# Kernel optimization log

Hardware: AMD Instinct MI355X
Metric: run time of the kernel (lower is better)

## Reference

```python
import jax, jax.numpy as jnp
import numpy as np


def setup_inputs() -> dict:
    key = jax.random.key(0)
    k1, k2, k3 = jax.random.split(key, 3)
    B, N, F = 32, 1024, 128
    x = jax.random.normal(k1, (B, N, F), dtype=jnp.float32)
    adj = jax.random.uniform(k2, (B, N, N), dtype=jnp.float32)
    # Linear(in_feature=128, out_feature=128) params (Kaiming-ish scale)
    W = jax.random.normal(k3, (F, F), dtype=jnp.float32) * (1.0 / np.sqrt(F))
    b = jnp.zeros((F,), dtype=jnp.float32)
    return {"x": x, "adj": adj, "W": W, "b": b}


def reference(x, adj, W, b):
    # h = W(x) ; dropout is identity in inference mode
    h = jnp.einsum("bnf,fg->bng", x, W) + b          # [B,N,F]
    h = jnp.einsum("bnm,bmf->bnf", adj, h)           # neighbor aggregation
    return jax.nn.relu(h + x)                          # residual + ReLU
```

## Files before the change

kernel.cpp:

```cpp
#include <hip/hip_runtime.h>
#include <stdint.h>

typedef unsigned short u16;
typedef __attribute__((ext_vector_type(4))) u16    u16x4;
typedef __attribute__((ext_vector_type(8))) u16    u16x8;
typedef __attribute__((ext_vector_type(4))) float  f32x4;
typedef __attribute__((ext_vector_type(8))) __bf16 bf16x8;

__device__ __forceinline__ u16 f2bf(float f) {
    union { float f; uint32_t u; } v; v.f = f;
    uint32_t u = v.u;
    uint32_t rb = 0x7FFFu + ((u >> 16) & 1u);
    return (u16)((u + rb) >> 16);
}

__global__ __launch_bounds__(256) void gcn_wt(const float* __restrict__ W,
                                              u16* __restrict__ Wt) {
    int idx = blockIdx.x * 256 + threadIdx.x;
    int k = idx >> 7, f = idx & 127;
    Wt[f * 128 + k] = f2bf(W[idx]);
}

__global__ __launch_bounds__(256) void gcn_xw(const float* __restrict__ x,
                                              const u16* __restrict__ Wt,
                                              const float* __restrict__ bias,
                                              u16* __restrict__ hT) {
    __shared__ u16 Wl[128 * 128];
    __shared__ u16 Xl[128 * 128];
    const int t  = threadIdx.x;
    const int bb = blockIdx.x >> 3;
    const int n0 = (blockIdx.x & 7) << 7;

#pragma unroll
    for (int i = 0; i < 16; ++i) {
        int o  = i * 256 + t;
        int f  = o >> 5;
        int kb = (o & 31) * 8;
        u16x4 v = *(const u16x4*)((const char*)Wt + o * 8);
        *(u16x4*)((char*)Wl + f * 256 + (kb ^ ((f & 7) << 4))) = v;
    }
    const float* xb = x + (size_t)bb * (1024 * 128) + (size_t)n0 * 128;
#pragma unroll
    for (int i = 0; i < 16; ++i) {
        int o4 = i * 256 + t;
        int n  = o4 >> 5;
        int kb = (o4 & 31) * 8;
        f32x4 v = *(const f32x4*)(xb + (size_t)o4 * 4);
        u16x4 h; h.x = f2bf(v.x); h.y = f2bf(v.y); h.z = f2bf(v.z); h.w = f2bf(v.w);
        *(u16x4*)((char*)Xl + n * 256 + (kb ^ ((n & 7) << 4))) = h;
    }
    __syncthreads();

    const int w = t >> 6, l = t & 63;
    const int wr = w >> 1, wc = w & 1;
    f32x4 acc[4][4] = {};
#pragma unroll
    for (int kk = 0; kk < 4; ++kk) {
        const int kbyte = kk * 64 + (l >> 4) * 16;
        bf16x8 a[4], b[4];
#pragma unroll
        for (int mf = 0; mf < 4; ++mf) {
            int fl = wr * 64 + mf * 16 + (l & 15);
            a[mf] = *(const bf16x8*)((const char*)Wl + fl * 256 + (kbyte ^ ((fl & 7) << 4)));
        }
#pragma unroll
        for (int nn = 0; nn < 4; ++nn) {
            int nl = wc * 64 + nn * 16 + (l & 15);
            b[nn] = *(const bf16x8*)((const char*)Xl + nl * 256 + (kbyte ^ ((nl & 7) << 4)));
        }
#pragma unroll
        for (int mf = 0; mf < 4; ++mf)
#pragma unroll
            for (int nn = 0; nn < 4; ++nn)
                acc[mf][nn] = __builtin_amdgcn_mfma_f32_16x16x32_bf16(
                    a[mf], b[nn], acc[mf][nn], 0, 0, 0);
    }

    u16* ho = hT + (size_t)bb * 131072;
#pragma unroll
    for (int mf = 0; mf < 4; ++mf) {
        int fbase = wr * 64 + mf * 16 + (l >> 4) * 4;
#pragma unroll
        for (int r = 0; r < 4; ++r) {
            float bv = bias[fbase + r];
#pragma unroll
            for (int nn = 0; nn < 4; ++nn) {
                int n = wc * 64 + nn * 16 + (l & 15);
                ho[(size_t)(fbase + r) * 1024 + n0 + n] = f2bf(acc[mf][nn][r] + bv);
            }
        }
    }
}

__global__ __launch_bounds__(256) void gcn_agg(const float* __restrict__ adj,
                                               const u16* __restrict__ hT,
                                               const float* __restrict__ x,
                                               float* __restrict__ out) {
    __shared__ u16 Al[64 * 64];
    __shared__ u16 Bl[128 * 64];

    const int t = threadIdx.x;
    const int L  = (blockIdx.x & 7) * 64 + (blockIdx.x >> 3);
    const int bb = L >> 4;
    const int r0 = (L & 15) << 6;

    const float* adjb = adj + (size_t)bb * 1024 * 1024 + (size_t)r0 * 1024;
    const u16*   hTb  = hT + (size_t)bb * 131072;

    const int w = t >> 6, l = t & 63;
    const int wr = w >> 1, wc = w & 1;
    f32x4 acc[2][4] = {};

    f32x4 aReg[4];
    u16x8 bReg[4];
#pragma unroll
    for (int i = 0; i < 4; ++i) {
        int o4 = i * 256 + t;
        aReg[i] = *(const f32x4*)(adjb + (size_t)(o4 >> 4) * 1024 + (o4 & 15) * 4);
        int o16 = i * 256 + t;
        bReg[i] = *(const u16x8*)((const char*)(hTb + (size_t)(o16 >> 3) * 1024) + (o16 & 7) * 16);
    }

    for (int ks = 0; ks < 16; ++ks) {
        if (ks) __syncthreads();
#pragma unroll
        for (int i = 0; i < 4; ++i) {
            int o4 = i * 256 + t;
            int r = o4 >> 4, kb = (o4 & 15) * 8;
            u16x4 h; h.x = f2bf(aReg[i].x); h.y = f2bf(aReg[i].y);
            h.z = f2bf(aReg[i].z); h.w = f2bf(aReg[i].w);
            *(u16x4*)((char*)Al + r * 128 + (kb ^ ((r & 7) << 4))) = h;
            int o16 = i * 256 + t;
            int f = o16 >> 3, kb2 = (o16 & 7) * 16;
            *(u16x8*)((char*)Bl + f * 128 + (kb2 ^ ((f & 7) << 4))) = bReg[i];
        }
        __syncthreads();

        if (ks + 1 < 16) {
            int k0n = (ks + 1) * 64;
#pragma unroll
            for (int i = 0; i < 4; ++i) {
                int o4 = i * 256 + t;
                aReg[i] = *(const f32x4*)(adjb + (size_t)(o4 >> 4) * 1024 + k0n + (o4 & 15) * 4);
                int o16 = i * 256 + t;
                bReg[i] = *(const u16x8*)((const char*)(hTb + (size_t)(o16 >> 3) * 1024 + k0n) + (o16 & 7) * 16);
            }
        }

#pragma unroll
        for (int kk = 0; kk < 2; ++kk) {
            const int kbyte = kk * 64 + (l >> 4) * 16;
            bf16x8 a[2], b[4];
#pragma unroll
            for (int mf = 0; mf < 2; ++mf) {
                int rl = wr * 32 + mf * 16 + (l & 15);
                a[mf] = *(const bf16x8*)((const char*)Al + rl * 128 + (kbyte ^ ((rl & 7) << 4)));
            }
#pragma unroll
            for (int nn = 0; nn < 4; ++nn) {
                int fl = wc * 64 + nn * 16 + (l & 15);
                b[nn] = *(const bf16x8*)((const char*)Bl + fl * 128 + (kbyte ^ ((fl & 7) << 4)));
            }
#pragma unroll
            for (int mf = 0; mf < 2; ++mf)
#pragma unroll
                for (int nn = 0; nn < 4; ++nn)
                    acc[mf][nn] = __builtin_amdgcn_mfma_f32_16x16x32_bf16(
                        a[mf], b[nn], acc[mf][nn], 0, 0, 0);
        }
    }

    const float* xb = x + (size_t)bb * 131072;
    float*       ob = out + (size_t)bb * 131072;
#pragma unroll
    for (int mf = 0; mf < 2; ++mf) {
#pragma unroll
        for (int j = 0; j < 4; ++j) {
            int r = r0 + wr * 32 + mf * 16 + (l >> 4) * 4 + j;
#pragma unroll
            for (int nn = 0; nn < 4; ++nn) {
                int f = wc * 64 + nn * 16 + (l & 15);
                size_t idx = (size_t)r * 128 + f;
                float v = acc[mf][nn][j] + xb[idx];
                ob[idx] = fmaxf(v, 0.0f);
            }
        }
    }
}

extern "C" void kernel_launch(void* const* d_in, const int* in_sizes, int n_in,
                              void* d_out, int out_size, void* d_ws, size_t ws_size,
                              hipStream_t stream) {
    const float* x    = (const float*)d_in[0];
    const float* adj  = (const float*)d_in[1];
    const float* W    = (const float*)d_in[2];
    const float* bias = (const float*)d_in[3];
    float* out = (float*)d_out;

    u16* hT = (u16*)d_ws;
    u16* Wt = (u16*)((char*)d_ws + (size_t)32 * 131072 * 2);

    gcn_wt <<<dim3(64),  dim3(256), 0, stream>>>(W, Wt);
    gcn_xw <<<dim3(256), dim3(256), 0, stream>>>(x, Wt, bias, hT);
    gcn_agg<<<dim3(512), dim3(256), 0, stream>>>(adj, hT, x, out);
}
```

Before: 40.54 us.

## Stream adj and hT directly to LDS with double-buffered async loads

The aggregation kernel now uses global_load_lds to copy fp32 adjacency tiles and bf16 hT tiles straight into double-buffered shared memory, using a pre-swizzled source addressing scheme. The fp32-to-bf16 conversion moves from the staging path to the fragment read just before the MFMA. This removes the register round trip and lets the next tile's load overlap compute. The cost is doubled LDS (fp32 adj tile plus two buffers), which may reduce occupancy, and conversion work is repeated per wave read.

```diff
diff --git a/kernel.cpp b/kernel.cpp
--- a/kernel.cpp
+++ b/kernel.cpp
@@ -12,6 +12,13 @@
     uint32_t u = v.u;
     uint32_t rb = 0x7FFFu + ((u >> 16) & 1u);
     return (u16)((u + rb) >> 16);
+}
+
+__device__ __forceinline__ bf16x8 cvt8(f32x4 a, f32x4 b) {
+    bf16x8 r;
+    r[0] = (__bf16)a.x; r[1] = (__bf16)a.y; r[2] = (__bf16)a.z; r[3] = (__bf16)a.w;
+    r[4] = (__bf16)b.x; r[5] = (__bf16)b.y; r[6] = (__bf16)b.z; r[7] = (__bf16)b.w;
+    return r;
 }
 
 __global__ __launch_bounds__(256) void gcn_wt(const float* __restrict__ W,
@@ -96,79 +103,91 @@
                                                const u16* __restrict__ hT,
                                                const float* __restrict__ x,
                                                float* __restrict__ out) {
-    __shared__ u16 Al[64 * 64];
-    __shared__ u16 Bl[128 * 64];
+    __shared__ float Al[2][64 * 64];
+    __shared__ u16   Bl[2][128 * 64];
 
     const int t = threadIdx.x;
     const int L  = (blockIdx.x & 7) * 64 + (blockIdx.x >> 3);
     const int bb = L >> 4;
     const int r0 = (L & 15) << 6;
 
-    const float* adjb = adj + (size_t)bb * 1024 * 1024 + (size_t)r0 * 1024;
+    const float* adjb = adj + (size_t)bb * 1048576 + (size_t)r0 * 1024;
     const u16*   hTb  = hT + (size_t)bb * 131072;
 
     const int w = t >> 6, l = t & 63;
     const int wr = w >> 1, wc = w & 1;
+
+    const float* srcA[4];
+    const u16*   srcB[4];
+#pragma unroll
+    for (int i = 0; i < 4; ++i) {
+        int c  = (w * 4 + i) * 64 + l;
+        int rA = c >> 4, cbA = ((c & 15) * 16) ^ ((rA & 7) << 4);
+        srcA[i] = adjb + (size_t)rA * 1024 + (cbA >> 2);
+        int fB = c >> 3, cbB = ((c & 7) * 16) ^ ((fB & 7) << 4);
+        srcB[i] = hTb + (size_t)fB * 1024 + (cbB >> 1);
+    }
+
+#define STAGE(buf, ks)                                                          \
+    do {                                                                        \
+        const int k0 = (ks) * 64;                                               \
+        _Pragma("unroll")                                                       \
+        for (int i = 0; i < 4; ++i) {                                           \
+            __builtin_amdgcn_global_load_lds(                                   \
+                (const __attribute__((address_space(1))) void*)(srcA[i] + k0),  \
+                (__attribute__((address_space(3))) void*)((char*)&Al[buf][0] + (w * 4 + i) * 1024), \
+                16, 0, 0);                                                      \
+            __builtin_amdgcn_global_load_lds(                                   \
+                (const __attribute__((address_space(1))) void*)(srcB[i] + k0),  \
+                (__attribute__((address_space(3))) void*)((char*)&Bl[buf][0] + (w * 4 + i) * 1024), \
+                16, 0, 0);                                                      \
+        }                                                                       \
+    } while (0)
+
+#define COMPUTE(buf)                                                            \
+    do {                                                                        \
+        _Pragma("unroll")                                                       \
+        for (int kk = 0; kk < 2; ++kk) {                                        \
+            const int ke = kk * 32 + (l >> 4) * 8;                              \
+            bf16x8 a[2], b[4];                                                  \
+            _Pragma("unroll")                                                   \
+            for (int mf = 0; mf < 2; ++mf) {                                    \
+                int rl  = wr * 32 + mf * 16 + (l & 15);                         \
+                int cb0 = (ke * 4) ^ ((rl & 7) << 4);                           \
+                int cb1 = (ke * 4 + 16) ^ ((rl & 7) << 4);                      \
+                f32x4 lo = *(const f32x4*)((const char*)&Al[buf][0] + rl * 256 + cb0); \
+                f32x4 hi = *(const f32x4*)((const char*)&Al[buf][0] + rl * 256 + cb1); \
+                a[mf] = cvt8(lo, hi);                                           \
+            }                                                                   \
+            _Pragma("unroll")                                                   \
+            for (int nn = 0; nn < 4; ++nn) {                                    \
+                int fl = wc * 64 + nn * 16 + (l & 15);                          \
+                int cb = (ke * 2) ^ ((fl & 7) << 4);                            \
+                b[nn] = *(const bf16x8*)((const char*)&Bl[buf][0] + fl * 128 + cb); \
+            }                                                                   \
+            _Pragma("unroll")                                                   \
+            for (int mf = 0; mf < 2; ++mf)                                      \
+                _Pragma("unroll")                                               \
+                for (int nn = 0; nn < 4; ++nn)                                  \
+                    acc[mf][nn] = __builtin_amdgcn_mfma_f32_16x16x32_bf16(      \
+                        a[mf], b[nn], acc[mf][nn], 0, 0, 0);                    \
+        }                                                                       \
+    } while (0)
+
     f32x4 acc[2][4] = {};
 
-    f32x4 aReg[4];
-    u16x8 bReg[4];
-#pragma unroll
-    for (int i = 0; i < 4; ++i) {
-        int o4 = i * 256 + t;
-        aReg[i] = *(const f32x4*)(adjb + (size_t)(o4 >> 4) * 1024 + (o4 & 15) * 4);
-        int o16 = i * 256 + t;
-        bReg[i] = *(const u16x8*)((const char*)(hTb + (size_t)(o16 >> 3) * 1024) + (o16 & 7) * 16);
-    }
-
-    for (int ks = 0; ks < 16; ++ks) {
-        if (ks) __syncthreads();
-#pragma unroll
-        for (int i = 0; i < 4; ++i) {
-            int o4 = i * 256 + t;
-            int r = o4 >> 4, kb = (o4 & 15) * 8;
-            u16x4 h; h.x = f2bf(aReg[i].x); h.y = f2bf(aReg[i].y);
-            h.z = f2bf(aReg[i].z); h.w = f2bf(aReg[i].w);
-            *(u16x4*)((char*)Al + r * 128 + (kb ^ ((r & 7) << 4))) = h;
-            int o16 = i * 256 + t;
-            int f = o16 >> 3, kb2 = (o16 & 7) * 16;
-            *(u16x8*)((char*)Bl + f * 128 + (kb2 ^ ((f & 7) << 4))) = bReg[i];
-        }
+    STAGE(0, 0);
+    __syncthreads();
+    for (int ks = 0; ks < 16; ks += 2) {
+        STAGE(1, ks + 1);
+        COMPUTE(0);
         __syncthreads();
-
-        if (ks + 1 < 16) {
-            int k0n = (ks + 1) * 64;
-#pragma unroll
-            for (int i = 0; i < 4; ++i) {
-                int o4 = i * 256 + t;
-                aReg[i] = *(const f32x4*)(adjb + (size_t)(o4 >> 4) * 1024 + k0n + (o4 & 15) * 4);
-                int o16 = i * 256 + t;
-                bReg[i] = *(const u16x8*)((const char*)(hTb + (size_t)(o16 >> 3) * 1024 + k0n) + (o16 & 7) * 16);
-            }
-        }
-
-#pragma unroll
-        for (int kk = 0; kk < 2; ++kk) {
-            const int kbyte = kk * 64 + (l >> 4) * 16;
-            bf16x8 a[2], b[4];
-#pragma unroll
-            for (int mf = 0; mf < 2; ++mf) {
-                int rl = wr * 32 + mf * 16 + (l & 15);
-                a[mf] = *(const bf16x8*)((const char*)Al + rl * 128 + (kbyte ^ ((rl & 7) << 4)));
-            }
-#pragma unroll
-            for (int nn = 0; nn < 4; ++nn) {
-                int fl = wc * 64 + nn * 16 + (l & 15);
-                b[nn] = *(const bf16x8*)((const char*)Bl + fl * 128 + (kbyte ^ ((fl & 7) << 4)));
-            }
-#pragma unroll
-            for (int mf = 0; mf < 2; ++mf)
-#pragma unroll
-                for (int nn = 0; nn < 4; ++nn)
-                    acc[mf][nn] = __builtin_amdgcn_mfma_f32_16x16x32_bf16(
-                        a[mf], b[nn], acc[mf][nn], 0, 0, 0);
-        }
-    }
+        if (ks + 2 < 16) STAGE(0, ks + 2);
+        COMPUTE(1);
+        __syncthreads();
+    }
+#undef STAGE
+#undef COMPUTE
 
     const float* xb = x + (size_t)bb * 131072;
     float*       ob = out + (size_t)bb * 131072;
```

After: 44.96 us. +10.9%, slower.

## Reassociate GCN as (adj·x)·W with bias via ones-row, fuse into one main kernel

Applied to the files above, without the earlier changes.

Reorders the computation to first aggregate adj·x (with an extra ones column giving row sums for the bias) and then apply W inside the same kernel, removing the separate x·W kernel and the hT intermediate. A prep kernel transposes x to bf16 and packs W with bias into an augmented layout. The main kernel streams adj straight from global memory into registers, with no LDS staging, and splits K across wave pairs that are reduced through LDS. This adds an extra bf16 rounding of the intermediate adj·x, which can change accuracy.

```diff
diff --git a/kernel.cpp b/kernel.cpp
--- a/kernel.cpp
+++ b/kernel.cpp
@@ -7,6 +7,8 @@
 typedef __attribute__((ext_vector_type(4))) float  f32x4;
 typedef __attribute__((ext_vector_type(8))) __bf16 bf16x8;
 
+union BF8 { u16x8 u; bf16x8 b; };
+
 __device__ __forceinline__ u16 f2bf(float f) {
     union { float f; uint32_t u; } v; v.f = f;
     uint32_t u = v.u;
@@ -14,177 +16,156 @@
     return (u16)((u + rb) >> 16);
 }
 
-__global__ __launch_bounds__(256) void gcn_wt(const float* __restrict__ W,
-                                              u16* __restrict__ Wt) {
-    int idx = blockIdx.x * 256 + threadIdx.x;
-    int k = idx >> 7, f = idx & 127;
-    Wt[f * 128 + k] = f2bf(W[idx]);
+__device__ __forceinline__ bf16x8 cvt8(f32x4 a, f32x4 b) {
+    bf16x8 r;
+    r[0] = (__bf16)a.x; r[1] = (__bf16)a.y; r[2] = (__bf16)a.z; r[3] = (__bf16)a.w;
+    r[4] = (__bf16)b.x; r[5] = (__bf16)b.y; r[6] = (__bf16)b.z; r[7] = (__bf16)b.w;
+    return r;
 }
 
-__global__ __launch_bounds__(256) void gcn_xw(const float* __restrict__ x,
-                                              const u16* __restrict__ Wt,
-                                              const float* __restrict__ bias,
-                                              u16* __restrict__ hT) {
-    __shared__ u16 Wl[128 * 128];
-    __shared__ u16 Xl[128 * 128];
-    const int t  = threadIdx.x;
-    const int bb = blockIdx.x >> 3;
-    const int n0 = (blockIdx.x & 7) << 7;
+__global__ __launch_bounds__(256) void gcn_prep(const float* __restrict__ x,
+                                                const float* __restrict__ W,
+                                                const float* __restrict__ bias,
+                                                u16* __restrict__ xT,
+                                                u16* __restrict__ WaTp) {
+    const int t = threadIdx.x;
+    if (blockIdx.x == 512) {
+#pragma unroll
+        for (int i = 0; i < 80; ++i) {
+            int idx = i * 256 + t;
+            int f = idx / 160, pp = idx % 160;
+            int c = pp >> 5, lg = (pp >> 3) & 3, jj = pp & 7;
+            int g = c * 32 + (jj < 4 ? lg * 4 + jj : 16 + lg * 4 + (jj - 4));
+            float v = (g < 128) ? W[(size_t)g * 128 + f]
+                                : (g == 128 ? bias[f] : 0.0f);
+            WaTp[f * 160 + pp] = f2bf(v);
+        }
+        return;
+    }
+    __shared__ u16 Xt[64 * 128];
+    const int bb = blockIdx.x >> 4;
+    const int n0 = (blockIdx.x & 15) << 6;
+    const float* xb = x + (size_t)bb * 131072 + (size_t)n0 * 128;
+#pragma unroll
+    for (int i = 0; i < 8; ++i) {
+        int o4 = i * 256 + t;
+        f32x4 v = *(const f32x4*)(xb + (size_t)o4 * 4);
+        u16x4 hv; hv.x = f2bf(v.x); hv.y = f2bf(v.y);
+        hv.z = f2bf(v.z); hv.w = f2bf(v.w);
+        *(u16x4*)(Xt + o4 * 4) = hv;
+    }
+    __syncthreads();
+    const int g = t >> 1, nh = (t & 1) * 32;
+    u16* dst = xT + (size_t)bb * 131072 + (size_t)g * 1024 + n0 + nh;
+#pragma unroll
+    for (int q = 0; q < 4; ++q) {
+        u16x8 v;
+#pragma unroll
+        for (int j = 0; j < 8; ++j) v[j] = Xt[(nh + q * 8 + j) * 128 + g];
+        *(u16x8*)(dst + q * 8) = v;
+    }
+}
+
+__global__ __launch_bounds__(512, 4)
+void gcn_main(const float* __restrict__ adj, const float* __restrict__ x,
+              const u16* __restrict__ xT, const u16* __restrict__ WaTp,
+              float* __restrict__ out) {
+    __shared__ f32x4 Plds[8 * 9 * 64];
+
+    const int t = threadIdx.x;
+    const int L   = (blockIdx.x & 7) * 64 + (blockIdx.x >> 3);
+    const int bb  = L >> 4;
+    const int r0b = (L & 15) << 6;
+    const int w = t >> 6, l = t & 63;
+    const int lc = l & 15, lg = l >> 4;
+    const int p = w >> 1, h = w & 1;
+    const int r0w = r0b + p * 16;
+
+    const float* adjRow = adj + (size_t)bb * 1048576 + (size_t)(r0w + lc) * 1024 + lg * 8;
+    const u16*   xTrow  = xT + (size_t)bb * 131072 + (size_t)lc * 1024 + lg * 8;
+
+    BF8 ones;
+    {
+        u16 o = (lc == 0) ? (u16)0x3F80 : (u16)0;
+#pragma unroll
+        for (int j = 0; j < 8; ++j) ones.u[j] = o;
+    }
+
+    f32x4 y2[9] = {};
+    const int ntBase = h * 512;
+
+    f32x4 a0 = *(const f32x4*)(adjRow + ntBase);
+    f32x4 a1 = *(const f32x4*)(adjRow + ntBase + 4);
+    u16x8 xc[8];
+#pragma unroll
+    for (int gt = 0; gt < 8; ++gt)
+        xc[gt] = *(const u16x8*)(xTrow + gt * 16384 + ntBase);
 
 #pragma unroll
     for (int i = 0; i < 16; ++i) {
-        int o  = i * 256 + t;
-        int f  = o >> 5;
-        int kb = (o & 31) * 8;
-        u16x4 v = *(const u16x4*)((const char*)Wt + o * 8);
-        *(u16x4*)((char*)Wl + f * 256 + (kb ^ ((f & 7) << 4))) = v;
-    }
-    const float* xb = x + (size_t)bb * (1024 * 128) + (size_t)n0 * 128;
+        const int nOff = ntBase + i * 32;
+        f32x4 na0, na1; u16x8 nx[8];
+        if (i < 15) {
+            na0 = *(const f32x4*)(adjRow + nOff + 32);
+            na1 = *(const f32x4*)(adjRow + nOff + 36);
 #pragma unroll
-    for (int i = 0; i < 16; ++i) {
-        int o4 = i * 256 + t;
-        int n  = o4 >> 5;
-        int kb = (o4 & 31) * 8;
-        f32x4 v = *(const f32x4*)(xb + (size_t)o4 * 4);
-        u16x4 h; h.x = f2bf(v.x); h.y = f2bf(v.y); h.z = f2bf(v.z); h.w = f2bf(v.w);
-        *(u16x4*)((char*)Xl + n * 256 + (kb ^ ((n & 7) << 4))) = h;
-    }
-    __syncthreads();
-
-    const int w = t >> 6, l = t & 63;
-    const int wr = w >> 1, wc = w & 1;
-    f32x4 acc[4][4] = {};
+            for (int gt = 0; gt < 8; ++gt)
+                nx[gt] = *(const u16x8*)(xTrow + gt * 16384 + nOff + 32);
+        }
+        BF8 bf; bf.b = cvt8(a0, a1);
 #pragma unroll
-    for (int kk = 0; kk < 4; ++kk) {
-        const int kbyte = kk * 64 + (l >> 4) * 16;
-        bf16x8 a[4], b[4];
+        for (int gt = 0; gt < 8; ++gt) {
+            BF8 xa; xa.u = xc[gt];
+            y2[gt] = __builtin_amdgcn_mfma_f32_16x16x32_bf16(xa.b, bf.b, y2[gt], 0, 0, 0);
+        }
+        y2[8] = __builtin_amdgcn_mfma_f32_16x16x32_bf16(ones.b, bf.b, y2[8], 0, 0, 0);
+        if (i < 15) {
+            a0 = na0; a1 = na1;
 #pragma unroll
-        for (int mf = 0; mf < 4; ++mf) {
-            int fl = wr * 64 + mf * 16 + (l & 15);
-            a[mf] = *(const bf16x8*)((const char*)Wl + fl * 256 + (kbyte ^ ((fl & 7) << 4)));
-        }
-#pragma unroll
-        for (int nn = 0; nn < 4; ++nn) {
-            int nl = wc * 64 + nn * 16 + (l & 15);
-            b[nn] = *(const bf16x8*)((const char*)Xl + nl * 256 + (kbyte ^ ((nl & 7) << 4)));
-        }
-#pragma unroll
-        for (int mf = 0; mf < 4; ++mf)
-#pragma unroll
-            for (int nn = 0; nn < 4; ++nn)
-                acc[mf][nn] = __builtin_amdgcn_mfma_f32_16x16x32_bf16(
-                    a[mf], b[nn], acc[mf][nn], 0, 0, 0);
-    }
-
-    u16* ho = hT + (size_t)bb * 131072;
-#pragma unroll
-    for (int mf = 0; mf < 4; ++mf) {
-        int fbase = wr * 64 + mf * 16 + (l >> 4) * 4;
-#pragma unroll
-        for (int r = 0; r < 4; ++r) {
-            float bv = bias[fbase + r];
-#pragma unroll
-            for (int nn = 0; nn < 4; ++nn) {
-                int n = wc * 64 + nn * 16 + (l & 15);
-                ho[(size_t)(fbase + r) * 1024 + n0 + n] = f2bf(acc[mf][nn][r] + bv);
-            }
-        }
-    }
-}
-
-__global__ __launch_bounds__(256) void gcn_agg(const float* __restrict__ adj,
-                                               const u16* __restrict__ hT,
-                                               const float* __restrict__ x,
-                                               float* __restrict__ out) {
-    __shared__ u16 Al[64 * 64];
-    __shared__ u16 Bl[128 * 64];
-
-    const int t = threadIdx.x;
-    const int L  = (blockIdx.x & 7) * 64 + (blockIdx.x >> 3);
-    const int bb = L >> 4;
-    const int r0 = (L & 15) << 6;
-
-    const float* adjb = adj + (size_t)bb * 1024 * 1024 + (size_t)r0 * 1024;
-    const u16*   hTb  = hT + (size_t)bb * 131072;
-
-    const int w = t >> 6, l = t & 63;
-    const int wr = w >> 1, wc = w & 1;
-    f32x4 acc[2][4] = {};
-
-    f32x4 aReg[4];
-    u16x8 bReg[4];
-#pragma unroll
-    for (int i = 0; i < 4; ++i) {
-        int o4 = i * 256 + t;
-        aReg[i] = *(const f32x4*)(adjb + (size_t)(o4 >> 4) * 1024 + (o4 & 15) * 4);
-        int o16 = i * 256 + t;
-        bReg[i] = *(const u16x8*)((const char*)(hTb + (size_t)(o16 >> 3) * 1024) + (o16 & 7) * 16);
-    }
-
-    for (int ks = 0; ks < 16; ++ks) {
-        if (ks) __syncthreads();
-#pragma unroll
-        for (int i = 0; i < 4; ++i) {
-            int o4 = i * 256 + t;
-            int r = o4 >> 4, kb = (o4 & 15) * 8;
-            u16x4 h; h.x = f2bf(aReg[i].x); h.y = f2bf(aReg[i].y);
-            h.z = f2bf(aReg[i].z); h.w = f2bf(aReg[i].w);
-            *(u16x4*)((char*)Al + r * 128 + (kb ^ ((r & 7) << 4))) = h;
-            int o16 = i * 256 + t;
-            int f = o16 >> 3, kb2 = (o16 & 7) * 16;
-            *(u16x8*)((char*)Bl + f * 128 + (kb2 ^ ((f & 7) << 4))) = bReg[i];
-        }
-        __syncthreads();
-
-        if (ks + 1 < 16) {
-            int k0n = (ks + 1) * 64;
-#pragma unroll
-            for (int i = 0; i < 4; ++i) {
-                int o4 = i * 256 + t;
-                aReg[i] = *(const f32x4*)(adjb + (size_t)(o4 >> 4) * 1024 + k0n + (o4 & 15) * 4);
-                int o16 = i * 256 + t;
-                bReg[i] = *(const u16x8*)((const char*)(hTb + (size_t)(o16 >> 3) * 1024 + k0n) + (o16 & 7) * 16);
-            }
-        }
-
-#pragma unroll
-        for (int kk = 0; kk < 2; ++kk) {
-            const int kbyte = kk * 64 + (l >> 4) * 16;
-            bf16x8 a[2], b[4];
-#pragma unroll
-            for (int mf = 0; mf < 2; ++mf) {
-                int rl = wr * 32 + mf * 16 + (l & 15);
-                a[mf] = *(const bf16x8*)((const char*)Al + rl * 128 + (kbyte ^ ((rl & 7) << 4)));
-            }
-#pragma unroll
-            for (int nn = 0; nn < 4; ++nn) {
-                int fl = wc * 64 + nn * 16 + (l & 15);
-                b[nn] = *(const bf16x8*)((const char*)Bl + fl * 128 + (kbyte ^ ((fl & 7) << 4)));
-            }
-#pragma unroll
-            for (int mf = 0; mf < 2; ++mf)
-#pragma unroll
-                for (int nn = 0; nn < 4; ++nn)
-                    acc[mf][nn] = __builtin_amdgcn_mfma_f32_16x16x32_bf16(
-                        a[mf], b[nn], acc[mf][nn], 0, 0, 0);
+            for (int gt = 0; gt < 8; ++gt) xc[gt] = nx[gt];
         }
     }
 
-    const float* xb = x + (size_t)bb * 131072;
-    float*       ob = out + (size_t)bb * 131072;
 #pragma unroll
-    for (int mf = 0; mf < 2; ++mf) {
+    for (int gt = 0; gt < 9; ++gt)
+        Plds[(w * 9 + gt) * 64 + l] = y2[gt];
+    __syncthreads();
+
+    f32x4 ys[9];
 #pragma unroll
-        for (int j = 0; j < 4; ++j) {
-            int r = r0 + wr * 32 + mf * 16 + (l >> 4) * 4 + j;
+    for (int gt = 0; gt < 9; ++gt)
+        ys[gt] = Plds[((p * 2) * 9 + gt) * 64 + l] +
+                 Plds[((p * 2 + 1) * 9 + gt) * 64 + l];
+
+    f32x4 z[4] = {};
 #pragma unroll
-            for (int nn = 0; nn < 4; ++nn) {
-                int f = wc * 64 + nn * 16 + (l & 15);
-                size_t idx = (size_t)r * 128 + f;
-                float v = acc[mf][nn][j] + xb[idx];
-                ob[idx] = fmaxf(v, 0.0f);
-            }
+    for (int c = 0; c < 5; ++c) {
+        BF8 breg;
+#pragma unroll
+        for (int jj = 0; jj < 4; ++jj) breg.b[jj] = (__bf16)ys[2 * c][jj];
+#pragma unroll
+        for (int jj = 0; jj < 4; ++jj)
+            breg.b[4 + jj] = (c < 4) ? (__bf16)ys[2 * c + 1][jj] : (__bf16)0.0f;
+#pragma unroll
+        for (int ft = 0; ft < 4; ++ft) {
+            int f = h * 64 + ft * 16 + lc;
+            BF8 aw;
+            aw.u = *(const u16x8*)(WaTp + f * 160 + c * 32 + lg * 8);
+            z[ft] = __builtin_amdgcn_mfma_f32_16x16x32_bf16(aw.b, breg.b, z[ft], 0, 0, 0);
         }
+    }
+
+    const int r = r0w + lc;
+    const float* xres = x + (size_t)bb * 131072 + (size_t)r * 128;
+    float*       ob   = out + (size_t)bb * 131072 + (size_t)r * 128;
+#pragma unroll
+    for (int ft = 0; ft < 4; ++ft) {
+        int fb = h * 64 + ft * 16 + lg * 4;
+        f32x4 xv = *(const f32x4*)(xres + fb);
+        f32x4 v;
+#pragma unroll
+        for (int j = 0; j < 4; ++j) v[j] = fmaxf(z[ft][j] + xv[j], 0.0f);
+        *(f32x4*)(ob + fb) = v;
     }
 }
 
@@ -197,10 +178,9 @@
     const float* bias = (const float*)d_in[3];
     float* out = (float*)d_out;
 
-    u16* hT = (u16*)d_ws;
-    u16* Wt = (u16*)((char*)d_ws + (size_t)32 * 131072 * 2);
+    u16* xT   = (u16*)d_ws;
+    u16* WaTp = (u16*)((char*)d_ws + (size_t)8 * 1024 * 1024);
 
-    gcn_wt <<<dim3(64),  dim3(256), 0, stream>>>(W, Wt);
-    gcn_xw <<<dim3(256), dim3(256), 0, stream>>>(x, Wt, bias, hT);
-    gcn_agg<<<dim3(512), dim3(256), 0, stream>>>(adj, hT, x, out);
+    gcn_prep<<<dim3(513), dim3(256), 0, stream>>>(x, W, bias, xT, WaTp);
+    gcn_main<<<dim3(512), dim3(512), 0, stream>>>(adj, x, xT, WaTp, out);
 }
```

Result: slower. 112.0 us (+176.2%).
